# Kernel tuning notes

Measured on AMD Instinct MI355X. Metric: run time of the kernel, lower is better.

## Reference

```python
import jax, jax.numpy as jnp
import numpy as np

T = 65536
DIN = 128
H = 128      # hidden_dim
L = 16       # latent_dim
NEG_SLOPE = 0.01  # flax nn.leaky_relu default


def _orth(key, shape, scale):
    a = jax.random.normal(key, shape, dtype=jnp.float32)
    q, r = jnp.linalg.qr(a if shape[0] >= shape[1] else a.T)
    q = q * jnp.sign(jnp.diag(r))
    q = q if shape[0] >= shape[1] else q.T
    return (scale * q[:shape[0], :shape[1]]).astype(jnp.float32)


def setup_inputs() -> dict:
    key = jax.random.key(0)
    ks = jax.random.split(key, 8)
    x = jax.random.normal(ks[0], (T, DIN), dtype=jnp.float32)
    mask = jax.random.bernoulli(ks[1], 0.9, (T,))
    W_in = _orth(ks[2], (DIN, H), float(np.sqrt(2.0)))
    b_in = jnp.zeros((H,), jnp.float32)
    # OptimizedLSTMCell params: input kernel [DIN_h, 4H], recurrent kernel [H, 4H], bias [4H]
    # gate order in flax: i, f, g, o
    Wi = jax.random.normal(ks[3], (H, 4 * H), dtype=jnp.float32) / np.sqrt(H)
    Wh = _orth(ks[4], (H, 4 * H), 1.0)
    b_lstm = jnp.zeros((4 * H,), jnp.float32)
    W_lat = _orth(ks[5], (H, L), 1.0)
    b_lat = jnp.zeros((L,), jnp.float32)
    return {"x": x, "mask": mask, "W_in": W_in, "b_in": b_in,
            "Wi": Wi, "Wh": Wh, "b_lstm": b_lstm,
            "W_lat": W_lat, "b_lat": b_lat}


def reference(x, mask, W_in, b_in, Wi, Wh, b_lstm, W_lat, b_lat):
    # input projection + leaky_relu
    xp = x @ W_in + b_in                      # [T, H]
    xp = jnp.where(xp >= 0, xp, NEG_SLOPE * xp)

    def step(carry, inp):
        c, h = carry
        xt, mt = inp
        z = xt @ Wi + h @ Wh + b_lstm         # [4H]
        i, f, g, o = jnp.split(z, 4)
        c_new = jax.nn.sigmoid(f) * c + jax.nn.sigmoid(i) * jnp.tanh(g)
        h_new = jax.nn.sigmoid(o) * jnp.tanh(c_new)
        # masked carry update: keep old carry where mask is False
        c2 = jnp.where(mt, c_new, c)
        h2 = jnp.where(mt, h_new, h)
        return (c2, h2), h_new

    init = (jnp.zeros((H,), xp.dtype), jnp.zeros((H,), xp.dtype))
    (c_f, h_f), _ = jax.lax.scan(step, init, (xp, mask))
    latent = h_f @ W_lat + b_lat              # [L]
    return latent
```

## Files before the change

### kernel.cpp

```cpp
#include <hip/hip_runtime.h>
#include <hip/hip_fp16.h>


#define TT   65536
#define DINN 128
#define HH   128
#define G4   512
#define NEG  0.01f
#define ROWS 16
#define CTH  1024

#define SC_SIG  (-1.4426950408889634f)
#define SC_TANH ( 2.8853900817779268f)

typedef _Float16 f16x8 __attribute__((ext_vector_type(8)));
typedef float    f32x4 __attribute__((ext_vector_type(4)));

#if defined(__has_builtin)
#if __has_builtin(__builtin_amdgcn_rcpf)
#define RCPF(x) __builtin_amdgcn_rcpf(x)
#endif
#if __has_builtin(__builtin_amdgcn_exp2f)
#define EXP2F(x) __builtin_amdgcn_exp2f(x)
#endif
#endif
#ifndef RCPF
#define RCPF(x) (1.0f / (x))
#endif
#ifndef EXP2F
#define EXP2F(x) exp2f(x)
#endif

#define MF16(a, b, c) __builtin_amdgcn_mfma_f32_16x16x32_f16((a), (b), (c), 0, 0, 0)

#define LDS_BARRIER() asm volatile("s_waitcnt lgkmcnt(0)\n\ts_barrier" ::: "memory")

__global__ __launch_bounds__(CTH) void compact_kernel(
    const int* __restrict__ mask, int* __restrict__ pos, int* __restrict__ cnt_out)
{
    __shared__ int sc[CTH];
    const int th   = threadIdx.x;
    const int base = th * (TT / CTH);
    int cnt = 0;
    #pragma unroll 8
    for (int k = 0; k < TT / CTH; ++k) cnt += (mask[base + k] != 0);
    sc[th] = cnt;
    __syncthreads();
    for (int off = 1; off < CTH; off <<= 1) {
        int v = sc[th];
        int u = (th >= off) ? sc[th - off] : 0;
        __syncthreads();
        sc[th] = v + u;
        __syncthreads();
    }
    int p = sc[th] - cnt;
    for (int k = 0; k < TT / CTH; ++k) {
        int t = base + k;
        pos[t] = p;
        p += (mask[t] != 0);
    }
    if (th == CTH - 1) cnt_out[0] = sc[CTH - 1];
}

__global__ __launch_bounds__(512) void zx_kernel(
    const float* __restrict__ x, const float* __restrict__ W_in,
    const float* __restrict__ b_in, const float* __restrict__ Wi,
    const float* __restrict__ b_lstm, const int* __restrict__ mask,
    const int* __restrict__ pos, __half* __restrict__ zc)
{
    __shared__ float xt[ROWS][DINN];
    __shared__ float xp[ROWS][DINN];
    const int tid = threadIdx.x;
    const int t0  = blockIdx.x * ROWS;

    {
        const float4* src = (const float4*)(x + (size_t)t0 * DINN);
        ((float4*)&xt[0][0])[tid] = src[tid];
    }
    __syncthreads();

    {
        const int c  = tid & 127;
        const int r0 = tid >> 7;
        float a0 = b_in[c], a1 = a0, a2 = a0, a3 = a0;
        #pragma unroll
        for (int k4 = 0; k4 < DINN / 4; ++k4) {
            const float w0 = W_in[(k4*4+0)*DINN + c];
            const float w1 = W_in[(k4*4+1)*DINN + c];
            const float w2 = W_in[(k4*4+2)*DINN + c];
            const float w3 = W_in[(k4*4+3)*DINN + c];
            float4 v0 = *(const float4*)&xt[r0 +  0][k4*4];
            float4 v1 = *(const float4*)&xt[r0 +  4][k4*4];
            float4 v2 = *(const float4*)&xt[r0 +  8][k4*4];
            float4 v3 = *(const float4*)&xt[r0 + 12][k4*4];
            a0 += v0.x*w0 + v0.y*w1 + v0.z*w2 + v0.w*w3;
            a1 += v1.x*w0 + v1.y*w1 + v1.z*w2 + v1.w*w3;
            a2 += v2.x*w0 + v2.y*w1 + v2.z*w2 + v2.w*w3;
            a3 += v3.x*w0 + v3.y*w1 + v3.z*w2 + v3.w*w3;
        }
        xp[r0 +  0][c] = a0 >= 0.f ? a0 : NEG * a0;
        xp[r0 +  4][c] = a1 >= 0.f ? a1 : NEG * a1;
        xp[r0 +  8][c] = a2 >= 0.f ? a2 : NEG * a2;
        xp[r0 + 12][c] = a3 >= 0.f ? a3 : NEG * a3;
    }
    __syncthreads();

    {
        const int c2 = tid;
        float acc[ROWS];
        const float bl = b_lstm[c2];
        #pragma unroll
        for (int r = 0; r < ROWS; ++r) acc[r] = bl;
        #pragma unroll 4
        for (int k4 = 0; k4 < DINN / 4; ++k4) {
            const float w0 = Wi[(k4*4+0)*G4 + c2];
            const float w1 = Wi[(k4*4+1)*G4 + c2];
            const float w2 = Wi[(k4*4+2)*G4 + c2];
            const float w3 = Wi[(k4*4+3)*G4 + c2];
            #pragma unroll
            for (int r = 0; r < ROWS; ++r) {
                float4 a = *(const float4*)&xp[r][k4*4];
                acc[r] += a.x*w0 + a.y*w1 + a.z*w2 + a.w*w3;
            }
        }
        const int   gate = c2 >> 7;
        const int   unit = c2 & 127;
        const int   dst  = (unit >> 5) * 128 + (unit & 15) * 8
                         + ((unit >> 4) & 1) * 4 + gate;
        const float gsc  = (gate == 2) ? SC_TANH : SC_SIG;
        #pragma unroll
        for (int r = 0; r < ROWS; ++r) {
            const int t = t0 + r;
            if (mask[t])
                zc[(size_t)pos[t] * G4 + dst] = __float2half(acc[r] * gsc);
        }
    }
}

#define DBW(g,a,kt) f16x8 bw##g##_##a##_##kt;
#define LBW(g,a,kt) { f16x8 v_;                                            \
    const float sc_ = ((g) == 2) ? SC_TANH : SC_SIG;                       \
    const int col_ = ((g) << 7) + (w << 5) + ((a) << 4) + li;              \
    _Pragma("unroll")                                                      \
    for (int j_ = 0; j_ < 8; ++j_)                                         \
        v_[j_] = (_Float16)(Wh[((kt)*32 + r8 + j_)*G4 + col_] * sc_);      \
    bw##g##_##a##_##kt = v_; }
#define PBW(g,a,kt) asm volatile("" : "+v"(bw##g##_##a##_##kt));

#define FORKT(M,g,a) M(g,a,0) M(g,a,1) M(g,a,2) M(g,a,3)
#define FORA(M,g)    FORKT(M,g,0) FORKT(M,g,1)
#define FORALLB(M)   FORA(M,0) FORA(M,1) FORA(M,2) FORA(M,3)

#define CHAIN(g,a,zout) {                                             \
    f32x4 d_ = MF16(af0, bw##g##_##a##_0, zq);                        \
    d_ = MF16(af1, bw##g##_##a##_1, d_);                              \
    d_ = MF16(af2, bw##g##_##a##_2, d_);                              \
    d_ = MF16(af3, bw##g##_##a##_3, d_);                              \
    (zout) = d_[0]; }

#define STEP(ZZ, PI, PO) {                                            \
    const __half2 zl = *(const __half2*)&(ZZ).x;                      \
    const __half2 zh = *(const __half2*)&(ZZ).y;                      \
    const __half* hb_ = hbuf[PI];                                     \
    const f16x8 af0 = *(const f16x8*)&hb_[ 0 + r8];                   \
    const f16x8 af1 = *(const f16x8*)&hb_[32 + r8];                   \
    const f16x8 af2 = *(const f16x8*)&hb_[64 + r8];                   \
    const f16x8 af3 = *(const f16x8*)&hb_[96 + r8];                   \
    float z00, z01, z10, z11, z20, z21, z30, z31;                     \
    CHAIN(0,0,z00) CHAIN(0,1,z01)                                     \
    CHAIN(1,0,z10) CHAIN(1,1,z11)                                     \
    CHAIN(2,0,z20) CHAIN(2,1,z21)                                     \
    CHAIN(3,0,z30) CHAIN(3,1,z31)                                     \
    const float zi = (asel ? z01 : z00) + __half2float(zl.x);         \
    const float zf = (asel ? z11 : z10) + __half2float(zl.y);         \
    const float zg = (asel ? z21 : z20) + __half2float(zh.x);         \
    const float zo = (asel ? z31 : z30) + __half2float(zh.y);         \
    const float i_s = RCPF(1.f + EXP2F(zi));                          \
    const float f_s = RCPF(1.f + EXP2F(zf));                          \
    const float o_s = RCPF(1.f + EXP2F(zo));                          \
    const float g_t = 1.f - 2.f * RCPF(EXP2F(zg) + 1.f);              \
    c_st = f_s * c_st + i_s * g_t;                                    \
    const float t_c = 1.f - 2.f * RCPF(EXP2F(SC_TANH * c_st) + 1.f);  \
    h_st = o_s * t_c;                                                 \
    if (wr) hbuf[PO][uout] = __float2half(h_st);                      \
    LDS_BARRIER();                                                    \
}

__global__ __launch_bounds__(256, 1)
__attribute__((amdgpu_waves_per_eu(1, 1)))
void scan_kernel(
    const __half* __restrict__ zc, const float* __restrict__ Wh,
    const int* __restrict__ cnt, const float* __restrict__ W_lat,
    const float* __restrict__ b_lat, float* __restrict__ out)
{
    const int n    = threadIdx.x;
    const int w    = n >> 6;
    const int lane = n & 63;
    const int li   = lane & 15;
    const int r    = lane >> 4;
    const int r8   = r << 3;
    const bool asel = (r & 1);
    const bool wr   = (r < 2);
    const int uout  = (w << 5) + (r << 4) + li;

    FORALLB(DBW)
    FORALLB(LBW)
    FORALLB(PBW)

    f32x4 zq = { 0.f, 0.f, 0.f, 0.f };
    asm volatile("" : "+v"(zq));

    __shared__ __align__(16) __half hbuf[2][HH];
    __shared__ float hfin[HH];
    ((__half*)hbuf)[n] = __float2half(0.f);
    float c_st = 0.f, h_st = 0.f;
    __syncthreads();

    const int S = cnt[0];
    const uint2* prow = (const uint2*)zc + (w << 5) + (li << 1) + (int)asel;
    uint2 z0 = prow[0];
    uint2 z1 = prow[128];
    prow += 256;

    int i = 0;
    for (; i + 1 < S; i += 2) {
        const uint2 za = prow[0];
        const uint2 zb = prow[128];
        prow += 256;
        STEP(z0, 0, 1)
        STEP(z1, 1, 0)
        z0 = za;
        z1 = zb;
    }
    if (i < S) {
        STEP(z0, 0, 1)
    }

    if (wr) hfin[uout] = h_st;
    __syncthreads();
    if (n < 16) {
        float acc = b_lat[n];
        #pragma unroll
        for (int k = 0; k < HH; ++k) acc += hfin[k] * W_lat[k * 16 + n];
        out[n] = acc;
    }
}

extern "C" void kernel_launch(void* const* d_in, const int* in_sizes, int n_in,
                              void* d_out, int out_size, void* d_ws, size_t ws_size,
                              hipStream_t stream) {
    const float* x      = (const float*)d_in[0];
    const int*   mask   = (const int*)  d_in[1];
    const float* W_in   = (const float*)d_in[2];
    const float* b_in   = (const float*)d_in[3];
    const float* Wi     = (const float*)d_in[4];
    const float* Wh     = (const float*)d_in[5];
    const float* b_lstm = (const float*)d_in[6];
    const float* W_lat  = (const float*)d_in[7];
    const float* b_lat  = (const float*)d_in[8];
    float* out = (float*)d_out;

    __half* zc  = (__half*)d_ws;
    int*    pos = (int*)((char*)d_ws + (size_t)(TT + 4) * G4 * 2);
    int*    cnt = pos + TT;

    compact_kernel<<<1, CTH, 0, stream>>>(mask, pos, cnt);
    zx_kernel<<<TT / ROWS, 512, 0, stream>>>(x, W_in, b_in, Wi, b_lstm,
                                             mask, pos, zc);
    scan_kernel<<<1, 256, 0, stream>>>(zc, Wh, cnt, W_lat, b_lat, out);
}
```

Baseline: 23.11 ms.

## Spread LSTM recurrent matvec across 8 waves with one unit group per wave

The sequential scan kernel now runs 512 threads (8 waves, two per SIMD) instead of 256, and each wave owns 16 hidden units. It computes 4 MFMA chains per step instead of 8, with no selection between two unit halves. The per-step zc layout is simplified to unit*4+gate to match. This halves the MFMA chain work per wave on the latency-bound recurrence. In exchange the per-step barrier now synchronises more waves, and two waves share each SIMD.

```diff
diff --git a/kernel.cpp b/kernel.cpp
--- a/kernel.cpp
+++ b/kernel.cpp
@@ -125,8 +125,7 @@
         }
         const int   gate = c2 >> 7;
         const int   unit = c2 & 127;
-        const int   dst  = (unit >> 5) * 128 + (unit & 15) * 8
-                         + ((unit >> 4) & 1) * 4 + gate;
+        const int   dst  = unit * 4 + gate;
         const float gsc  = (gate == 2) ? SC_TANH : SC_SIG;
         #pragma unroll
         for (int r = 0; r < ROWS; ++r) {
@@ -137,25 +136,24 @@
     }
 }
 
-#define DBW(g,a,kt) f16x8 bw##g##_##a##_##kt;
-#define LBW(g,a,kt) { f16x8 v_;                                            \
+#define DBW(g,kt) f16x8 bw##g##_##kt;
+#define LBW(g,kt) { f16x8 v_;                                              \
     const float sc_ = ((g) == 2) ? SC_TANH : SC_SIG;                       \
-    const int col_ = ((g) << 7) + (w << 5) + ((a) << 4) + li;              \
+    const int col_ = ((g) << 7) + u16 + li;                                \
     _Pragma("unroll")                                                      \
     for (int j_ = 0; j_ < 8; ++j_)                                         \
         v_[j_] = (_Float16)(Wh[((kt)*32 + r8 + j_)*G4 + col_] * sc_);      \
-    bw##g##_##a##_##kt = v_; }
-#define PBW(g,a,kt) asm volatile("" : "+v"(bw##g##_##a##_##kt));
-
-#define FORKT(M,g,a) M(g,a,0) M(g,a,1) M(g,a,2) M(g,a,3)
-#define FORA(M,g)    FORKT(M,g,0) FORKT(M,g,1)
-#define FORALLB(M)   FORA(M,0) FORA(M,1) FORA(M,2) FORA(M,3)
-
-#define CHAIN(g,a,zout) {                                             \
-    f32x4 d_ = MF16(af0, bw##g##_##a##_0, zq);                        \
-    d_ = MF16(af1, bw##g##_##a##_1, d_);                              \
-    d_ = MF16(af2, bw##g##_##a##_2, d_);                              \
-    d_ = MF16(af3, bw##g##_##a##_3, d_);                              \
+    bw##g##_##kt = v_; }
+#define PBW(g,kt) asm volatile("" : "+v"(bw##g##_##kt));
+
+#define FORKT(M,g) M(g,0) M(g,1) M(g,2) M(g,3)
+#define FORALLB(M) FORKT(M,0) FORKT(M,1) FORKT(M,2) FORKT(M,3)
+
+#define CHAIN(g,zout) {                                               \
+    f32x4 d_ = MF16(af0, bw##g##_0, zq);                              \
+    d_ = MF16(af1, bw##g##_1, d_);                                    \
+    d_ = MF16(af2, bw##g##_2, d_);                                    \
+    d_ = MF16(af3, bw##g##_3, d_);                                    \
     (zout) = d_[0]; }
 
 #define STEP(ZZ, PI, PO) {                                            \
@@ -166,15 +164,12 @@
     const f16x8 af1 = *(const f16x8*)&hb_[32 + r8];                   \
     const f16x8 af2 = *(const f16x8*)&hb_[64 + r8];                   \
     const f16x8 af3 = *(const f16x8*)&hb_[96 + r8];                   \
-    float z00, z01, z10, z11, z20, z21, z30, z31;                     \
-    CHAIN(0,0,z00) CHAIN(0,1,z01)                                     \
-    CHAIN(1,0,z10) CHAIN(1,1,z11)                                     \
-    CHAIN(2,0,z20) CHAIN(2,1,z21)                                     \
-    CHAIN(3,0,z30) CHAIN(3,1,z31)                                     \
-    const float zi = (asel ? z01 : z00) + __half2float(zl.x);         \
-    const float zf = (asel ? z11 : z10) + __half2float(zl.y);         \
-    const float zg = (asel ? z21 : z20) + __half2float(zh.x);         \
-    const float zo = (asel ? z31 : z30) + __half2float(zh.y);         \
+    float z0v, z1v, z2v, z3v;                                         \
+    CHAIN(0, z0v) CHAIN(1, z1v) CHAIN(2, z2v) CHAIN(3, z3v)           \
+    const float zi = z0v + __half2float(zl.x);                        \
+    const float zf = z1v + __half2float(zl.y);                        \
+    const float zg = z2v + __half2float(zh.x);                        \
+    const float zo = z3v + __half2float(zh.y);                        \
     const float i_s = RCPF(1.f + EXP2F(zi));                          \
     const float f_s = RCPF(1.f + EXP2F(zf));                          \
     const float o_s = RCPF(1.f + EXP2F(zo));                          \
@@ -182,26 +177,24 @@
     c_st = f_s * c_st + i_s * g_t;                                    \
     const float t_c = 1.f - 2.f * RCPF(EXP2F(SC_TANH * c_st) + 1.f);  \
     h_st = o_s * t_c;                                                 \
-    if (wr) hbuf[PO][uout] = __float2half(h_st);                      \
+    if (r == 0) hbuf[PO][u16 + li] = __float2half(h_st);              \
     LDS_BARRIER();                                                    \
 }
 
-__global__ __launch_bounds__(256, 1)
-__attribute__((amdgpu_waves_per_eu(1, 1)))
+__global__ __launch_bounds__(512, 2)
+__attribute__((amdgpu_waves_per_eu(2, 2)))
 void scan_kernel(
     const __half* __restrict__ zc, const float* __restrict__ Wh,
     const int* __restrict__ cnt, const float* __restrict__ W_lat,
     const float* __restrict__ b_lat, float* __restrict__ out)
 {
     const int n    = threadIdx.x;
-    const int w    = n >> 6;
+    const int wv   = n >> 6;
+    const int u16  = wv << 4;
     const int lane = n & 63;
     const int li   = lane & 15;
     const int r    = lane >> 4;
     const int r8   = r << 3;
-    const bool asel = (r & 1);
-    const bool wr   = (r < 2);
-    const int uout  = (w << 5) + (r << 4) + li;
 
     FORALLB(DBW)
     FORALLB(LBW)
@@ -212,12 +205,12 @@
 
     __shared__ __align__(16) __half hbuf[2][HH];
     __shared__ float hfin[HH];
-    ((__half*)hbuf)[n] = __float2half(0.f);
+    if (n < 256) ((__half*)hbuf)[n] = __float2half(0.f);
     float c_st = 0.f, h_st = 0.f;
     __syncthreads();
 
     const int S = cnt[0];
-    const uint2* prow = (const uint2*)zc + (w << 5) + (li << 1) + (int)asel;
+    const uint2* prow = (const uint2*)zc + u16 + li;
     uint2 z0 = prow[0];
     uint2 z1 = prow[128];
     prow += 256;
@@ -236,7 +229,7 @@
         STEP(z0, 0, 1)
     }
 
-    if (wr) hfin[uout] = h_st;
+    if (r == 0) hfin[u16 + li] = h_st;
     __syncthreads();
     if (n < 16) {
         float acc = b_lat[n];
@@ -267,5 +260,5 @@
     compact_kernel<<<1, CTH, 0, stream>>>(mask, pos, cnt);
     zx_kernel<<<TT / ROWS, 512, 0, stream>>>(x, W_in, b_in, Wi, b_lstm,
                                              mask, pos, zc);
-    scan_kernel<<<1, 256, 0, stream>>>(zc, Wh, cnt, W_lat, b_lat, out);
-}
+    scan_kernel<<<1, 512, 0, stream>>>(zc, Wh, cnt, W_lat, b_lat, out);
+}
```

New measurement: 25.49 ms. +10.3%, slower.
